# Kernel tuning notes

Hardware: AMD Instinct MI355X
Metric: run time of the kernel (lower is better)

The kernel has to match this reference:

```python
import jax, jax.numpy as jnp
import numpy as np

B = 2; S, H, W = 14, 28, 28; C = 128; NH = 8; WS = 7; SH = 3
N = WS ** 3            # 343 tokens per window
HID = 4 * C            # 512 MLP hidden
EPS = 1e-5
SCALE = (C // NH) ** -0.5


def _rel_index():
    # reproduces the torch code exactly (meshgrid indexing='xy', quirky strides)
    coords = np.stack(np.meshgrid(np.arange(WS), np.arange(WS), np.arange(WS), indexing='xy'))  # (3,7,7,7)
    flat = coords.reshape(3, -1)                              # (3, N)
    rel = flat[:, :, None] - flat[:, None, :]                 # (3, N, N)
    rel = rel.transpose(1, 2, 0).astype(np.int64)             # (N, N, 3)
    rel[..., 0] += WS - 1
    rel[..., 1] += WS - 1
    rel[..., 2] += WS - 1
    rel[..., 0] *= 3 * WS - 1
    rel[..., 1] *= 2 * WS - 1
    return rel.sum(-1)                                        # (N, N)


def _attn_mask():
    # standard shifted-window mask: 0 where same region, -100 otherwise
    img = np.zeros((S, H, W), np.float32)
    sl = (slice(0, -WS), slice(-WS, -SH), slice(-SH, None))
    cnt = 0
    for a in sl:
        for b in sl:
            for c in sl:
                img[a, b, c] = cnt
                cnt += 1
    mw = img.reshape(S // WS, WS, H // WS, WS, W // WS, WS)
    mw = mw.transpose(0, 2, 4, 1, 3, 5).reshape(-1, N)        # (nW, N)
    am = mw[:, None, :] - mw[:, :, None]
    return jnp.asarray(np.where(am != 0, -100.0, 0.0).astype(np.float32))


def setup_inputs() -> dict:
    key = jax.random.key(0)
    ks = jax.random.split(key, 8)
    rn = lambda k, shp, s=0.02: jax.random.normal(k, shp, jnp.float32) * s
    return {
        'x': jax.random.normal(ks[0], (B, S * H * W, C), jnp.float32),
        'mask_matrix': _attn_mask(),
        'g1': jnp.ones((C,), jnp.float32), 'b1': jnp.zeros((C,), jnp.float32),
        'qkv_w': rn(ks[1], (C, 3 * C)), 'qkv_b': jnp.zeros((3 * C,), jnp.float32),
        'rpb': rn(ks[2], ((2 * WS - 1) ** 3, NH)),
        'proj_w': rn(ks[3], (C, C)), 'proj_b': jnp.zeros((C,), jnp.float32),
        'g2': jnp.ones((C,), jnp.float32), 'b2': jnp.zeros((C,), jnp.float32),
        'fc1_w': rn(ks[4], (C, HID)), 'fc1_b': jnp.zeros((HID,), jnp.float32),
        'fc2_w': rn(ks[5], (HID, C)), 'fc2_b': jnp.zeros((C,), jnp.float32),
        'rel_index': jnp.asarray(_rel_index(), jnp.int32),
    }


def _ln(x, g, b):
    mu = x.mean(-1, keepdims=True)
    d = x - mu
    var = (d * d).mean(-1, keepdims=True)
    return d * jax.lax.rsqrt(var + EPS) * g + b


def reference(x, mask_matrix, g1, b1, qkv_w, qkv_b, rpb, proj_w, proj_b,
              g2, b2, fc1_w, fc1_b, fc2_w, fc2_b, rel_index):
    shortcut = x
    h = _ln(x, g1, b1).reshape(B, S, H, W, C)
    h = jnp.roll(h, (-SH, -SH, -SH), axis=(1, 2, 3))
    # window partition -> (B_, N, C)
    h = h.reshape(B, S // WS, WS, H // WS, WS, W // WS, WS, C)
    h = h.transpose(0, 1, 3, 5, 2, 4, 6, 7).reshape(-1, N, C)
    B_ = h.shape[0]
    qkv = (h @ qkv_w + qkv_b).reshape(B_, N, 3, NH, C // NH).transpose(2, 0, 3, 1, 4)
    q, k, v = qkv[0] * SCALE, qkv[1], qkv[2]
    attn = jnp.einsum('bhnd,bhmd->bhnm', q, k)                # (B_, NH, N, N)
    bias = rpb[rel_index.reshape(-1)].reshape(N, N, NH).transpose(2, 0, 1)
    attn = attn + bias[None]
    nW = mask_matrix.shape[0]
    attn = attn.reshape(B_ // nW, nW, NH, N, N) + mask_matrix[None, :, None]
    attn = jax.nn.softmax(attn.reshape(B_, NH, N, N), axis=-1)
    o = jnp.einsum('bhnm,bhmd->bnhd', attn, v).reshape(B_, N, C)
    o = o @ proj_w + proj_b
    # window reverse -> (B, S, H, W, C)
    o = o.reshape(B, S // WS, H // WS, W // WS, WS, WS, WS, C)
    o = o.transpose(0, 1, 4, 2, 5, 3, 6, 7).reshape(B, S, H, W, C)
    o = jnp.roll(o, (SH, SH, SH), axis=(1, 2, 3)).reshape(B, S * H * W, C)
    x = shortcut + o
    y = _ln(x, g2, b2)
    y = jax.nn.gelu(y @ fc1_w + fc1_b, approximate=False) @ fc2_w + fc2_b
    return x + y
```

## Files before the change

kernel.cpp:

```cpp
#include <hip/hip_runtime.h>
#include <hip/hip_bf16.h>
#include <math.h>

typedef _Float16 half2_t __attribute__((ext_vector_type(2)));
typedef _Float16 half4_t __attribute__((ext_vector_type(4)));
typedef _Float16 half8_t __attribute__((ext_vector_type(8)));
typedef float float4_t __attribute__((ext_vector_type(4)));

#define MFMA16(a,b,c) __builtin_amdgcn_mfma_f32_16x16x16f16((a),(b),(c),0,0,0)
#define MFMA32(a,b,c) __builtin_amdgcn_mfma_f32_16x16x32_f16((a),(b),(c),0,0,0)

static __device__ __forceinline__ half2_t cvt_pk(float a, float b) {
  return __builtin_bit_cast(half2_t, __builtin_amdgcn_cvt_pkrtz(a, b));
}

static constexpr int NTOK = 21952;
static constexpr int NREG = 5488;
static constexpr float LOG2E = 1.44269504088896340736f;

__device__ __forceinline__ int rid_of(int cls, int n) {
  int z = n / 49, r = n - z*49, y = r / 7, x = r - y*7;
  int rs = (cls & 4) ? (z < 4 ? 1 : 2) : 0;
  int rh = (cls & 2) ? (y < 4 ? 1 : 2) : 0;
  int rw = (cls & 1) ? (x < 4 ? 1 : 2) : 0;
  return rs*9 + rh*3 + rw;
}

__global__ __launch_bounds__(256) void k_precomp(
    const float* __restrict__ qkv_w, const float* __restrict__ proj_w,
    const float* __restrict__ fc1_w, const float* __restrict__ fc2_w,
    const float* __restrict__ rpb,
    _Float16* __restrict__ qkv_wT, _Float16* __restrict__ proj_wT,
    _Float16* __restrict__ fc1_wT, _Float16* __restrict__ fc2_wT,
    _Float16* __restrict__ biasT, unsigned* __restrict__ bmask)
{
  int i = blockIdx.x * 256 + threadIdx.x;
  if (i < 49152) { int n = i >> 7, k = i & 127; qkv_wT[i] = (_Float16)qkv_w[k*384 + n]; return; }
  i -= 49152;
  if (i < 16384) { int n = i >> 7, k = i & 127; proj_wT[i] = (_Float16)proj_w[k*128 + n]; return; }
  i -= 16384;
  if (i < 65536) { int n = i >> 7, k = i & 127; fc1_wT[i] = (_Float16)fc1_w[k*512 + n]; return; }
  i -= 65536;
  if (i < 65536) { int n = i >> 9, k = i & 511; fc2_wT[i] = (_Float16)fc2_w[k*128 + n]; return; }
  i -= 65536;
  if (i < 8*343*352) {
    int h = i / (343*352); int r = i - h*343*352; int q = r / 352; int k = r - q*352;
    _Float16 v;
    if (k >= 343) v = (_Float16)(-30000.f);
    else {
      int zq = q/49, rq_ = q - zq*49, yq = rq_/7, xq = rq_ - yq*7;
      int zk = k/49, rk_ = k - zk*49, yk = rk_/7, xk = rk_ - yk*7;
      int idx = 20*(yq - yk + 6) + 13*(zq - zk + 6) + (xq - xk + 6);
      v = (_Float16)(rpb[idx*8 + h] * LOG2E);
    }
    biasT[i] = v;
    return;
  }
  i -= 8*343*352;
  if (i < 8*343*11) {
    int cls = i / (343*11); int r = i - cls*343*11; int q = r / 11; int kt = r - q*11;
    int rq = rid_of(cls, q);
    unsigned wbits = 0u;
    for (int j = 0; j < 32; ++j) {
      int k = kt*32 + j;
      if (k < 343 && rid_of(cls, k) == rq) wbits |= (1u << j);
    }
    bmask[i] = wbits;
  }
}

__device__ __forceinline__ void qkv_store(int row, int col, float v,
    const float* __restrict__ bias, _Float16* __restrict__ outh)
{
  v += bias[col];
  int which = col >> 7;
  if (which == 0) v *= 0.25f;
  int hh = (col >> 4) & 7, d = col & 15;
  int w = row / 343, n = row - w*343;
  size_t base = (size_t)((which*64 + w)*8 + hh)*NREG;
  if (which == 2) outh[base + d*343 + n] = (_Float16)v;
  else            outh[base + n*16  + d] = (_Float16)v;
}

__global__ __launch_bounds__(384) void k_qkv(
    const float* __restrict__ x, const float* __restrict__ g1, const float* __restrict__ b1,
    const _Float16* __restrict__ qkv_wT, const float* __restrict__ qkv_b,
    _Float16* __restrict__ qkvb)
{
  __shared__ _Float16 A[32][136];
  int mt = blockIdx.x;
  int tid = threadIdx.x, wid = tid >> 6, lane = tid & 63;
  for (int r = wid; r < 32; r += 6) {
    int row = mt*32 + r;
    int w = row / 343, n = row - w*343;
    int b = w >> 5, widx = w & 31;
    int sz = widx >> 4, sy = (widx >> 2) & 3, sx = widx & 3;
    int z = n / 49, rem = n - z*49, y = rem / 7, xx = rem - y*7;
    int gs = sz*7 + z + 3;  if (gs >= 14) gs -= 14;
    int gh = sy*7 + y + 3;  if (gh >= 28) gh -= 28;
    int gw = sx*7 + xx + 3; if (gw >= 28) gw -= 28;
    int gt = b*10976 + (gs*28 + gh)*28 + gw;
    const float* xr = x + (size_t)gt*128;
    float2 v = *(const float2*)(xr + lane*2);
    float s = v.x + v.y, sq = v.x*v.x + v.y*v.y;
    #pragma unroll
    for (int o = 1; o < 64; o <<= 1) { s += __shfl_xor(s, o); sq += __shfl_xor(sq, o); }
    float mu = s * 0.0078125f;
    float rstd = rsqrtf(sq*0.0078125f - mu*mu + 1e-5f);
    int c = lane*2;
    half2_t hv = { (_Float16)((v.x-mu)*rstd*g1[c]   + b1[c]),
                   (_Float16)((v.y-mu)*rstd*g1[c+1] + b1[c+1]) };
    *(half2_t*)&A[r][c] = hv;
  }
  __syncthreads();
  int lo = lane & 15, grp = lane >> 4;
  const _Float16* bp = qkv_wT + (size_t)(wid*64 + lo)*128 + grp*8;
  float4_t a00={0,0,0,0}, a01={0,0,0,0}, a02={0,0,0,0}, a03={0,0,0,0};
  float4_t a10={0,0,0,0}, a11={0,0,0,0}, a12={0,0,0,0}, a13={0,0,0,0};
  #pragma unroll
  for (int kk = 0; kk < 128; kk += 32) {
    half8_t f0 = *(const half8_t*)&A[lo][kk + grp*8];
    half8_t f1 = *(const half8_t*)&A[16 + lo][kk + grp*8];
    half8_t b0 = *(const half8_t*)(bp + kk);
    half8_t b1 = *(const half8_t*)(bp + kk + (size_t)16*128);
    half8_t b2 = *(const half8_t*)(bp + kk + (size_t)32*128);
    half8_t b3 = *(const half8_t*)(bp + kk + (size_t)48*128);
    a00 = MFMA32(f0, b0, a00);  a01 = MFMA32(f0, b1, a01);
    a02 = MFMA32(f0, b2, a02);  a03 = MFMA32(f0, b3, a03);
    a10 = MFMA32(f1, b0, a10);  a11 = MFMA32(f1, b1, a11);
    a12 = MFMA32(f1, b2, a12);  a13 = MFMA32(f1, b3, a13);
  }
  int row0 = mt*32 + grp*4;
  int colb = wid*64 + lo;
  #pragma unroll
  for (int r = 0; r < 4; ++r) {
    qkv_store(row0+r,    colb,    a00[r], qkv_b, qkvb);
    qkv_store(row0+r,    colb+16, a01[r], qkv_b, qkvb);
    qkv_store(row0+r,    colb+32, a02[r], qkv_b, qkvb);
    qkv_store(row0+r,    colb+48, a03[r], qkv_b, qkvb);
    qkv_store(row0+16+r, colb,    a10[r], qkv_b, qkvb);
    qkv_store(row0+16+r, colb+16, a11[r], qkv_b, qkvb);
    qkv_store(row0+16+r, colb+32, a12[r], qkv_b, qkvb);
    qkv_store(row0+16+r, colb+48, a13[r], qkv_b, qkvb);
  }
}

__global__ __launch_bounds__(512) void k_attn(
    const _Float16* __restrict__ qkv, const _Float16* __restrict__ biasT,
    const unsigned* __restrict__ bmask, _Float16* __restrict__ obuf)
{
  __shared__ _Float16 Klds[352][24];
  __shared__ _Float16 VTlds[16][360];
  int bx = blockIdx.x;
  int w = bx >> 3, h = bx & 7;
  int b = w >> 5, widx = w & 31;
  int sz = widx >> 4, sy = (widx >> 2) & 3, sx = widx & 3;
  int cls = (sz << 2) | (sy == 3 ? 2 : 0) | (sx == 3 ? 1 : 0);
  int tid = threadIdx.x;
  const _Float16* qp  = qkv + (size_t)(w*8 + h) * NREG;
  const _Float16* kp  = qp + (size_t)512  * NREG;
  const _Float16* vtp = qp + (size_t)1024 * NREG;
  for (int c = tid; c < 704; c += 512) {
    int n = c >> 1, d0 = (c & 1) * 8;
    half8_t kv = {};
    if (n < 343) kv = *(const half8_t*)(kp + n*16 + d0);
    *(half8_t*)&Klds[n][d0] = kv;
  }
  for (int c = tid; c < 704; c += 512) {
    int d = c / 44, n0 = (c - d*44) * 8;
    half8_t vv = {};
    if (n0 + 8 <= 343) vv = *(const half8_t*)(vtp + d*343 + n0);
    else { for (int j = 0; j < 8; ++j) vv[j] = (n0 + j < 343) ? vtp[d*343 + n0 + j] : (_Float16)0.f; }
    *(half8_t*)&VTlds[d][n0] = vv;
  }
  __syncthreads();
  int lane = tid & 63, lo = lane & 15, grp = lane >> 4;
  int wid = tid >> 6;
  for (int qt = wid; qt < 22; qt += 8) {
    int q  = qt*16 + lo;
    int qv = q < 343 ? q : 342;
    half4_t qf = *(const half4_t*)(qp + (size_t)qv*16 + grp*4);
    const _Float16* bp  = biasT + (size_t)(h*343 + qv)*352;
    const unsigned* bmp = bmask + (size_t)(cls*343 + qv)*11;
    half4_t barr0[11], barr1[11];
    unsigned bmarr[11];
    #pragma unroll
    for (int kt = 0; kt < 11; ++kt) {
      barr0[kt] = *(const half4_t*)(bp + kt*32 + grp*4);
      barr1[kt] = *(const half4_t*)(bp + kt*32 + 16 + grp*4);
      bmarr[kt] = bmp[kt];
    }
    float lsum = 0.f;
    float4_t acc = {0.f, 0.f, 0.f, 0.f};
    #pragma unroll
    for (int kt = 0; kt < 11; ++kt) {
      int kb = kt*32;
      half4_t ka0 = *(const half4_t*)&Klds[kb + lo][grp*4];
      half4_t ka1 = *(const half4_t*)&Klds[kb + 16 + lo][grp*4];
      float4_t zero = {0.f, 0.f, 0.f, 0.f};
      float4_t s0 = MFMA16(ka0, qf, zero);
      float4_t s1 = MFMA16(ka1, qf, zero);
      unsigned bmw = bmarr[kt];
      float p[8];
      #pragma unroll
      for (int i = 0; i < 8; ++i) {
        float sv = (i < 4) ? s0[i] : s1[i-4];
        float bb = (float)((i < 4) ? barr0[kt][i] : barr1[kt][i-4]);
        float e = exp2f(fmaf(sv, LOG2E, bb));
        unsigned bit = (bmw >> ((i >> 2)*16 + grp*4 + (i & 3))) & 1u;
        p[i] = bit ? e : 0.f;
        lsum += p[i];
      }
      half2_t pk01 = cvt_pk(p[0], p[1]);
      half2_t pk23 = cvt_pk(p[2], p[3]);
      half2_t pk45 = cvt_pk(p[4], p[5]);
      half2_t pk67 = cvt_pk(p[6], p[7]);
      half4_t pb0 = __builtin_shufflevector(pk01, pk23, 0, 1, 2, 3);
      half4_t pb1 = __builtin_shufflevector(pk45, pk67, 0, 1, 2, 3);
      half4_t va0 = *(const half4_t*)&VTlds[lo][kb + grp*4];
      half4_t va1 = *(const half4_t*)&VTlds[lo][kb + 16 + grp*4];
      acc = MFMA16(va0, pb0, acc);
      acc = MFMA16(va1, pb1, acc);
    }
    lsum += __shfl_xor(lsum, 16);
    lsum += __shfl_xor(lsum, 32);
    if (q < 343) {
      int z = q/49, rem = q - z*49, y = rem/7, xx = rem - y*7;
      int gs = sz*7 + z + 3;  if (gs >= 14) gs -= 14;
      int gh = sy*7 + y + 3;  if (gh >= 28) gh -= 28;
      int gw = sx*7 + xx + 3; if (gw >= 28) gw -= 28;
      int gt = b*10976 + (gs*28 + gh)*28 + gw;
      float rl = 1.f / lsum;
      half4_t o4 = { (_Float16)(acc[0]*rl), (_Float16)(acc[1]*rl),
                     (_Float16)(acc[2]*rl), (_Float16)(acc[3]*rl) };
      *(half4_t*)(obuf + (size_t)gt*128 + h*16 + grp*4) = o4;
    }
  }
}

__global__ __launch_bounds__(512) void k_mlp(
    const _Float16* __restrict__ obuf, const _Float16* __restrict__ proj_wT,
    const float* __restrict__ proj_b, const float* __restrict__ x,
    const float* __restrict__ g2, const float* __restrict__ b2,
    const _Float16* __restrict__ fc1_wT, const float* __restrict__ fc1_b,
    const _Float16* __restrict__ fc2_wT, const float* __restrict__ fc2_b,
    float* __restrict__ out)
{
  __shared__ _Float16 P[32][136];
  __shared__ _Float16 X2[32][136];
  __shared__ _Float16 H[32][520];
  int mt = blockIdx.x;
  int tid = threadIdx.x, wid = tid >> 6, lane = tid & 63, lo = lane & 15, grp = lane >> 4;
  for (int r = wid; r < 32; r += 8) {
    int row = mt*32 + r;
    half2_t v = *(const half2_t*)(obuf + (size_t)row*128 + lane*2);
    *(half2_t*)&P[r][lane*2] = v;
  }
  __syncthreads();
  {
    const _Float16* bp = proj_wT + (size_t)(wid*16 + lo)*128 + grp*8;
    half8_t wreg[4];
    #pragma unroll
    for (int k4 = 0; k4 < 4; ++k4) wreg[k4] = *(const half8_t*)(bp + k4*32);
    float4_t a0={0,0,0,0}, a1={0,0,0,0};
    #pragma unroll
    for (int k4 = 0; k4 < 4; ++k4) {
      half8_t f0 = *(const half8_t*)&P[lo][k4*32 + grp*8];
      half8_t f1 = *(const half8_t*)&P[16 + lo][k4*32 + grp*8];
      a0 = MFMA32(f0, wreg[k4], a0);
      a1 = MFMA32(f1, wreg[k4], a1);
    }
    int colb = wid*16 + lo;
    float bb = proj_b[colb];
    #pragma unroll
    for (int r = 0; r < 4; ++r) {
      int r0 = grp*4 + r;
      int row0 = mt*32 + r0, row1 = row0 + 16;
      X2[r0][colb]    = (_Float16)(x[(size_t)row0*128 + colb] + a0[r] + bb);
      X2[r0+16][colb] = (_Float16)(x[(size_t)row1*128 + colb] + a1[r] + bb);
    }
  }
  __syncthreads();
  for (int r = wid; r < 32; r += 8) {
    half2_t hx = *(const half2_t*)&X2[r][lane*2];
    float2 v = { (float)hx[0], (float)hx[1] };
    float s = v.x + v.y, sq = v.x*v.x + v.y*v.y;
    #pragma unroll
    for (int o = 1; o < 64; o <<= 1) { s += __shfl_xor(s, o); sq += __shfl_xor(sq, o); }
    float mu = s * 0.0078125f;
    float rstd = rsqrtf(sq*0.0078125f - mu*mu + 1e-5f);
    int c = lane*2;
    half2_t hv = { (_Float16)((v.x-mu)*rstd*g2[c]   + b2[c]),
                   (_Float16)((v.y-mu)*rstd*g2[c+1] + b2[c+1]) };
    *(half2_t*)&P[r][c] = hv;
  }
  __syncthreads();
  {
    const _Float16* bp = fc1_wT + (size_t)(wid*64 + lo)*128 + grp*8;
    half8_t w1[4][4];
    #pragma unroll
    for (int k4 = 0; k4 < 4; ++k4)
      #pragma unroll
      for (int j = 0; j < 4; ++j)
        w1[k4][j] = *(const half8_t*)(bp + k4*32 + (size_t)(j*16)*128);
    float4_t a00={0,0,0,0}, a01={0,0,0,0}, a02={0,0,0,0}, a03={0,0,0,0};
    float4_t a10={0,0,0,0}, a11={0,0,0,0}, a12={0,0,0,0}, a13={0,0,0,0};
    #pragma unroll
    for (int k4 = 0; k4 < 4; ++k4) {
      half8_t f0 = *(const half8_t*)&P[lo][k4*32 + grp*8];
      half8_t f1 = *(const half8_t*)&P[16 + lo][k4*32 + grp*8];
      a00 = MFMA32(f0, w1[k4][0], a00);  a01 = MFMA32(f0, w1[k4][1], a01);
      a02 = MFMA32(f0, w1[k4][2], a02);  a03 = MFMA32(f0, w1[k4][3], a03);
      a10 = MFMA32(f1, w1[k4][0], a10);  a11 = MFMA32(f1, w1[k4][1], a11);
      a12 = MFMA32(f1, w1[k4][2], a12);  a13 = MFMA32(f1, w1[k4][3], a13);
    }
    int colb = wid*64 + lo;
    #pragma unroll
    for (int r = 0; r < 4; ++r) {
      float vv[8] = { a00[r], a01[r], a02[r], a03[r], a10[r], a11[r], a12[r], a13[r] };
      #pragma unroll
      for (int j = 0; j < 8; ++j) {
        int rr  = grp*4 + r + (j >= 4 ? 16 : 0);
        int col = colb + (j & 3)*16;
        float v = vv[j] + fc1_b[col];
        float g = 0.5f * v * (1.0f + erff(v * 0.70710678118654752f));
        H[rr][col] = (_Float16)g;
      }
    }
  }
  __syncthreads();
  {
    const _Float16* bp = fc2_wT + (size_t)(wid*16 + lo)*512 + grp*8;
    half8_t w2[16];
    #pragma unroll
    for (int k = 0; k < 16; ++k) w2[k] = *(const half8_t*)(bp + k*32);
    float4_t c0={0,0,0,0}, c1={0,0,0,0};
    #pragma unroll
    for (int k = 0; k < 16; ++k) {
      half8_t f0 = *(const half8_t*)&H[lo][k*32 + grp*8];
      half8_t f1 = *(const half8_t*)&H[16 + lo][k*32 + grp*8];
      c0 = MFMA32(f0, w2[k], c0);
      c1 = MFMA32(f1, w2[k], c1);
    }
    int colb = wid*16 + lo;
    float bb = fc2_b[colb];
    #pragma unroll
    for (int r = 0; r < 4; ++r) {
      int r0 = grp*4 + r;
      int row0 = mt*32 + r0;
      out[(size_t)row0*128 + colb]      = (float)X2[r0][colb]    + c0[r] + bb;
      out[(size_t)(row0+16)*128 + colb] = (float)X2[r0+16][colb] + c1[r] + bb;
    }
  }
}

extern "C" void kernel_launch(void* const* d_in, const int* in_sizes, int n_in,
                              void* d_out, int out_size, void* d_ws, size_t ws_size,
                              hipStream_t stream)
{
  const float* x      = (const float*)d_in[0];
  const float* g1     = (const float*)d_in[2];
  const float* b1     = (const float*)d_in[3];
  const float* qkv_w  = (const float*)d_in[4];
  const float* qkv_b  = (const float*)d_in[5];
  const float* rpb    = (const float*)d_in[6];
  const float* proj_w = (const float*)d_in[7];
  const float* proj_b = (const float*)d_in[8];
  const float* g2     = (const float*)d_in[9];
  const float* b2     = (const float*)d_in[10];
  const float* fc1_w  = (const float*)d_in[11];
  const float* fc1_b  = (const float*)d_in[12];
  const float* fc2_w  = (const float*)d_in[13];
  const float* fc2_b  = (const float*)d_in[14];
  char* ws = (char*)d_ws;
  size_t o = 0;
  auto alloc = [&](size_t bytes) { size_t r = o; o += (bytes + 255) & ~size_t(255); return r; };
  size_t oOB  = alloc((size_t)NTOK*128*2);
  size_t oU   = alloc((size_t)NTOK*512*2);
  size_t oWQ  = alloc(49152*2);
  size_t oWP  = alloc(16384*2);
  size_t oW1  = alloc(65536*2);
  size_t oW2  = alloc(65536*2);
  size_t oBT  = alloc((size_t)8*343*352*2);
  size_t oBM  = alloc((size_t)8*343*11*4);
  (void)ws_size; (void)in_sizes; (void)n_in; (void)out_size;
  _Float16* obuf   = (_Float16*)(ws + oOB);
  _Float16* qkvb   = (_Float16*)(ws + oU);
  _Float16* qkv_wT = (_Float16*)(ws + oWQ);
  _Float16* proj_wT= (_Float16*)(ws + oWP);
  _Float16* fc1_wT = (_Float16*)(ws + oW1);
  _Float16* fc2_wT = (_Float16*)(ws + oW2);
  _Float16* biasT  = (_Float16*)(ws + oBT);
  unsigned* bmask  = (unsigned*)(ws + oBM);
  float*    out    = (float*)d_out;

  k_precomp<<<4662, 256, 0, stream>>>(qkv_w, proj_w, fc1_w, fc2_w, rpb,
                                      qkv_wT, proj_wT, fc1_wT, fc2_wT, biasT, bmask);
  k_qkv<<<686, 384, 0, stream>>>(x, g1, b1, qkv_wT, qkv_b, qkvb);
  k_attn<<<512, 512, 0, stream>>>(qkvb, biasT, bmask, obuf);
  k_mlp<<<686, 512, 0, stream>>>(obuf, proj_wT, proj_b, x, g2, b2,
                                 fc1_wT, fc1_b, fc2_wT, fc2_b, out);
}
```

Before: 106.4 us.

## Process 64 rows per MLP block and keep residual in output buffer

The MLP kernel now handles 64 tokens per block instead of 32, halving the grid and reusing the loaded projection weights across four row tiles. The fc1/fc2 stage runs twice over 32-row halves and reloads those weights per half. The post-attention residual is written to the output in fp32 and then accumulated with +=, which drops the separate X2 shared buffer and keeps the skip connection in fp32. The risks are the extra global read-modify-write on the output and lower occupancy with only 343 blocks.

```diff
diff --git a/kernel.cpp b/kernel.cpp
--- a/kernel.cpp
+++ b/kernel.cpp
@@ -246,43 +246,48 @@
     const _Float16* __restrict__ fc2_wT, const float* __restrict__ fc2_b,
     float* __restrict__ out)
 {
-  __shared__ _Float16 P[32][136];
-  __shared__ _Float16 X2[32][136];
+  __shared__ _Float16 P[64][136];
   __shared__ _Float16 H[32][520];
   int mt = blockIdx.x;
+  int row0b = mt*64;
   int tid = threadIdx.x, wid = tid >> 6, lane = tid & 63, lo = lane & 15, grp = lane >> 4;
-  for (int r = wid; r < 32; r += 8) {
-    int row = mt*32 + r;
-    half2_t v = *(const half2_t*)(obuf + (size_t)row*128 + lane*2);
+  for (int r = wid; r < 64; r += 8) {
+    half2_t v = *(const half2_t*)(obuf + (size_t)(row0b + r)*128 + lane*2);
     *(half2_t*)&P[r][lane*2] = v;
   }
   __syncthreads();
   {
     const _Float16* bp = proj_wT + (size_t)(wid*16 + lo)*128 + grp*8;
-    half8_t wreg[4];
-    #pragma unroll
-    for (int k4 = 0; k4 < 4; ++k4) wreg[k4] = *(const half8_t*)(bp + k4*32);
-    float4_t a0={0,0,0,0}, a1={0,0,0,0};
+    half8_t w[4];
+    #pragma unroll
+    for (int k4 = 0; k4 < 4; ++k4) w[k4] = *(const half8_t*)(bp + k4*32);
+    float4_t a[4] = { {0,0,0,0}, {0,0,0,0}, {0,0,0,0}, {0,0,0,0} };
     #pragma unroll
     for (int k4 = 0; k4 < 4; ++k4) {
-      half8_t f0 = *(const half8_t*)&P[lo][k4*32 + grp*8];
-      half8_t f1 = *(const half8_t*)&P[16 + lo][k4*32 + grp*8];
-      a0 = MFMA32(f0, wreg[k4], a0);
-      a1 = MFMA32(f1, wreg[k4], a1);
-    }
+      #pragma unroll
+      for (int j = 0; j < 4; ++j) {
+        half8_t f = *(const half8_t*)&P[j*16 + lo][k4*32 + grp*8];
+        a[j] = MFMA32(f, w[k4], a[j]);
+      }
+    }
+    __syncthreads();
     int colb = wid*16 + lo;
     float bb = proj_b[colb];
     #pragma unroll
-    for (int r = 0; r < 4; ++r) {
-      int r0 = grp*4 + r;
-      int row0 = mt*32 + r0, row1 = row0 + 16;
-      X2[r0][colb]    = (_Float16)(x[(size_t)row0*128 + colb] + a0[r] + bb);
-      X2[r0+16][colb] = (_Float16)(x[(size_t)row1*128 + colb] + a1[r] + bb);
+    for (int j = 0; j < 4; ++j) {
+      #pragma unroll
+      for (int r = 0; r < 4; ++r) {
+        int rr = j*16 + grp*4 + r;
+        int row = row0b + rr;
+        float val = x[(size_t)row*128 + colb] + a[j][r] + bb;
+        out[(size_t)row*128 + colb] = val;
+        P[rr][colb] = (_Float16)val;
+      }
     }
   }
   __syncthreads();
-  for (int r = wid; r < 32; r += 8) {
-    half2_t hx = *(const half2_t*)&X2[r][lane*2];
+  for (int r = wid; r < 64; r += 8) {
+    half2_t hx = *(const half2_t*)&P[r][lane*2];
     float2 v = { (float)hx[0], (float)hx[1] };
     float s = v.x + v.y, sq = v.x*v.x + v.y*v.y;
     #pragma unroll
@@ -295,62 +300,67 @@
     *(half2_t*)&P[r][c] = hv;
   }
   __syncthreads();
-  {
-    const _Float16* bp = fc1_wT + (size_t)(wid*64 + lo)*128 + grp*8;
-    half8_t w1[4][4];
-    #pragma unroll
-    for (int k4 = 0; k4 < 4; ++k4)
-      #pragma unroll
-      for (int j = 0; j < 4; ++j)
-        w1[k4][j] = *(const half8_t*)(bp + k4*32 + (size_t)(j*16)*128);
-    float4_t a00={0,0,0,0}, a01={0,0,0,0}, a02={0,0,0,0}, a03={0,0,0,0};
-    float4_t a10={0,0,0,0}, a11={0,0,0,0}, a12={0,0,0,0}, a13={0,0,0,0};
-    #pragma unroll
-    for (int k4 = 0; k4 < 4; ++k4) {
-      half8_t f0 = *(const half8_t*)&P[lo][k4*32 + grp*8];
-      half8_t f1 = *(const half8_t*)&P[16 + lo][k4*32 + grp*8];
-      a00 = MFMA32(f0, w1[k4][0], a00);  a01 = MFMA32(f0, w1[k4][1], a01);
-      a02 = MFMA32(f0, w1[k4][2], a02);  a03 = MFMA32(f0, w1[k4][3], a03);
-      a10 = MFMA32(f1, w1[k4][0], a10);  a11 = MFMA32(f1, w1[k4][1], a11);
-      a12 = MFMA32(f1, w1[k4][2], a12);  a13 = MFMA32(f1, w1[k4][3], a13);
-    }
-    int colb = wid*64 + lo;
-    #pragma unroll
-    for (int r = 0; r < 4; ++r) {
-      float vv[8] = { a00[r], a01[r], a02[r], a03[r], a10[r], a11[r], a12[r], a13[r] };
-      #pragma unroll
-      for (int j = 0; j < 8; ++j) {
-        int rr  = grp*4 + r + (j >= 4 ? 16 : 0);
-        int col = colb + (j & 3)*16;
-        float v = vv[j] + fc1_b[col];
-        float g = 0.5f * v * (1.0f + erff(v * 0.70710678118654752f));
-        H[rr][col] = (_Float16)g;
-      }
-    }
-  }
-  __syncthreads();
-  {
-    const _Float16* bp = fc2_wT + (size_t)(wid*16 + lo)*512 + grp*8;
-    half8_t w2[16];
-    #pragma unroll
-    for (int k = 0; k < 16; ++k) w2[k] = *(const half8_t*)(bp + k*32);
-    float4_t c0={0,0,0,0}, c1={0,0,0,0};
-    #pragma unroll
-    for (int k = 0; k < 16; ++k) {
-      half8_t f0 = *(const half8_t*)&H[lo][k*32 + grp*8];
-      half8_t f1 = *(const half8_t*)&H[16 + lo][k*32 + grp*8];
-      c0 = MFMA32(f0, w2[k], c0);
-      c1 = MFMA32(f1, w2[k], c1);
-    }
-    int colb = wid*16 + lo;
-    float bb = fc2_b[colb];
-    #pragma unroll
-    for (int r = 0; r < 4; ++r) {
-      int r0 = grp*4 + r;
-      int row0 = mt*32 + r0;
-      out[(size_t)row0*128 + colb]      = (float)X2[r0][colb]    + c0[r] + bb;
-      out[(size_t)(row0+16)*128 + colb] = (float)X2[r0+16][colb] + c1[r] + bb;
-    }
+  #pragma unroll
+  for (int half = 0; half < 2; ++half) {
+    int rb = half*32;
+    {
+      const _Float16* bp = fc1_wT + (size_t)(wid*64 + lo)*128 + grp*8;
+      half8_t w1[4][4];
+      #pragma unroll
+      for (int k4 = 0; k4 < 4; ++k4)
+        #pragma unroll
+        for (int j = 0; j < 4; ++j)
+          w1[k4][j] = *(const half8_t*)(bp + k4*32 + (size_t)(j*16)*128);
+      float4_t a00={0,0,0,0}, a01={0,0,0,0}, a02={0,0,0,0}, a03={0,0,0,0};
+      float4_t a10={0,0,0,0}, a11={0,0,0,0}, a12={0,0,0,0}, a13={0,0,0,0};
+      #pragma unroll
+      for (int k4 = 0; k4 < 4; ++k4) {
+        half8_t f0 = *(const half8_t*)&P[rb + lo][k4*32 + grp*8];
+        half8_t f1 = *(const half8_t*)&P[rb + 16 + lo][k4*32 + grp*8];
+        a00 = MFMA32(f0, w1[k4][0], a00);  a01 = MFMA32(f0, w1[k4][1], a01);
+        a02 = MFMA32(f0, w1[k4][2], a02);  a03 = MFMA32(f0, w1[k4][3], a03);
+        a10 = MFMA32(f1, w1[k4][0], a10);  a11 = MFMA32(f1, w1[k4][1], a11);
+        a12 = MFMA32(f1, w1[k4][2], a12);  a13 = MFMA32(f1, w1[k4][3], a13);
+      }
+      int colb = wid*64 + lo;
+      #pragma unroll
+      for (int r = 0; r < 4; ++r) {
+        float vv[8] = { a00[r], a01[r], a02[r], a03[r], a10[r], a11[r], a12[r], a13[r] };
+        #pragma unroll
+        for (int j = 0; j < 8; ++j) {
+          int rr  = grp*4 + r + (j >= 4 ? 16 : 0);
+          int col = colb + (j & 3)*16;
+          float v = vv[j] + fc1_b[col];
+          float g = 0.5f * v * (1.0f + erff(v * 0.70710678118654752f));
+          H[rr][col] = (_Float16)g;
+        }
+      }
+    }
+    __syncthreads();
+    {
+      const _Float16* bp = fc2_wT + (size_t)(wid*16 + lo)*512 + grp*8;
+      half8_t w2[16];
+      #pragma unroll
+      for (int k = 0; k < 16; ++k) w2[k] = *(const half8_t*)(bp + k*32);
+      float4_t c0={0,0,0,0}, c1={0,0,0,0};
+      #pragma unroll
+      for (int k = 0; k < 16; ++k) {
+        half8_t f0 = *(const half8_t*)&H[lo][k*32 + grp*8];
+        half8_t f1 = *(const half8_t*)&H[16 + lo][k*32 + grp*8];
+        c0 = MFMA32(f0, w2[k], c0);
+        c1 = MFMA32(f1, w2[k], c1);
+      }
+      int colb = wid*16 + lo;
+      float bb = fc2_b[colb];
+      #pragma unroll
+      for (int r = 0; r < 4; ++r) {
+        int row0 = row0b + rb + grp*4 + r;
+        int row1 = row0 + 16;
+        out[(size_t)row0*128 + colb] += c0[r] + bb;
+        out[(size_t)row1*128 + colb] += c1[r] + bb;
+      }
+    }
+    __syncthreads();
   }
 }
 
@@ -398,6 +408,6 @@
                                       qkv_wT, proj_wT, fc1_wT, fc2_wT, biasT, bmask);
   k_qkv<<<686, 384, 0, stream>>>(x, g1, b1, qkv_wT, qkv_b, qkvb);
   k_attn<<<512, 512, 0, stream>>>(qkvb, biasT, bmask, obuf);
-  k_mlp<<<686, 512, 0, stream>>>(obuf, proj_wT, proj_b, x, g2, b2,
+  k_mlp<<<343, 512, 0, stream>>>(obuf, proj_wT, proj_b, x, g2, b2,
                                  fc1_wT, fc1_b, fc2_wT, fc2_b, out);
 }
```

New measurement: 115.1 us. 1.08x slower.
